# Optimization experiments

Measured on AMD Instinct MI355X. Metric: run time of the kernel, lower is better.

Reference implementation:

```python
import jax, jax.numpy as jnp
import numpy as np

B, c, H, W = 64, 3, 512, 512
R = 8  # region_num
C = B * c

def setup_inputs() -> dict:
    key = jax.random.key(0)
    k1, k2, k3 = jax.random.split(key, 3)
    return {
        "x": jax.random.normal(k1, (B, c, H, W), dtype=jnp.float32),
        "region_percentiles": jax.random.uniform(k2, (C * (R - 1),), dtype=jnp.float32),
        "proxy_percentiles": jax.random.uniform(k3, (C * R,), dtype=jnp.float32),
        "region_num": R,
    }

def reference(x, region_percentiles, proxy_percentiles, region_num):
    Bx, cx, Hx, Wx = x.shape
    Cx = Bx * cx
    xf = x.reshape(Cx, Hx * Wx)                       # (C, HW)
    min_val = xf.min(axis=1)                          # (C,)
    max_val = xf.max(axis=1)                          # (C,)
    # random percentile boundary positions per channel, sorted
    pos = (region_percentiles.reshape(Cx, region_num - 1)
           * (max_val - min_val)[:, None] + min_val[:, None])
    pos_sorted = jnp.sort(pos, axis=1)                # (C, R-1)
    # region ends: left = [min, pos...], right = [pos..., max + 1e-6]
    left = jnp.concatenate([min_val[:, None], pos_sorted], axis=1)          # (C, R)
    right = jnp.concatenate([pos_sorted, max_val[:, None] + 1e-6], axis=1)  # (C, R)
    # region id for each pixel: number of boundaries <= x (== argmax of inside-mask)
    ids = jax.vmap(lambda bnd, v: jnp.searchsorted(bnd, v, side='right'))(pos_sorted, xf)  # (C, HW) int32
    # random value inside each region, then gather per pixel
    rand_vals = left + proxy_percentiles.reshape(Cx, region_num) * (right - left)  # (C, R)
    proxy = jnp.take_along_axis(rand_vals, ids, axis=1)                            # (C, HW)
    return proxy.reshape(Bx, cx, Hx, Wx).astype(x.dtype)
```

## Files before the change

### kernel.cpp

```cpp
#include <hip/hip_runtime.h>
#include <math.h>

#pragma clang fp contract(off)

#define CCH   192
#define HW    (512*512)
#define RNUM  8
#define SPLIT 8

typedef float f32x4 __attribute__((ext_vector_type(4)));

__device__ __forceinline__ float mul_rn(float a, float b) {
    float r; asm volatile("v_mul_f32 %0, %1, %2" : "=v"(r) : "v"(a), "v"(b)); return r;
}
__device__ __forceinline__ float add_rn(float a, float b) {
    float r; asm volatile("v_add_f32 %0, %1, %2" : "=v"(r) : "v"(a), "v"(b)); return r;
}
__device__ __forceinline__ float sub_rn(float a, float b) {
    float r; asm volatile("v_sub_f32 %0, %1, %2" : "=v"(r) : "v"(a), "v"(b)); return r;
}

__global__ __launch_bounds__(256) void k_minmax(const float* __restrict__ x,
                                                float* __restrict__ ws) {
    __shared__ float smn[256], smx[256];
    const int chan = blockIdx.x / SPLIT;
    const int part = blockIdx.x % SPLIT;
    const int n4   = HW / 4 / SPLIT;

    const f32x4* px = (const f32x4*)(x + (size_t)chan * HW) + (size_t)part * n4;

    float mn = INFINITY, mx = -INFINITY;
    for (int i = threadIdx.x; i < n4; i += 256) {
        f32x4 v = px[i];
        mn = fminf(mn, fminf(fminf(v.x, v.y), fminf(v.z, v.w)));
        mx = fmaxf(mx, fmaxf(fmaxf(v.x, v.y), fmaxf(v.z, v.w)));
    }
    smn[threadIdx.x] = mn;
    smx[threadIdx.x] = mx;
    __syncthreads();
    for (int s = 128; s > 0; s >>= 1) {
        if (threadIdx.x < s) {
            smn[threadIdx.x] = fminf(smn[threadIdx.x], smn[threadIdx.x + s]);
            smx[threadIdx.x] = fmaxf(smx[threadIdx.x], smx[threadIdx.x + s]);
        }
        __syncthreads();
    }
    if (threadIdx.x == 0) {
        ws[(size_t)blockIdx.x * 2 + 0] = smn[0];
        ws[(size_t)blockIdx.x * 2 + 1] = smx[0];
    }
}

#define BLOCKS_PER_CH 16
__global__ __launch_bounds__(256) void k_apply(const float* __restrict__ x,
                                               const float* __restrict__ ws_part,
                                               const float* __restrict__ region_percentiles,
                                               const float* __restrict__ proxy_percentiles,
                                               float* __restrict__ out) {
    const int chan = blockIdx.x / BLOCKS_PER_CH;
    const int blk  = blockIdx.x % BLOCKS_PER_CH;
    const int n4   = HW / 4 / BLOCKS_PER_CH;

    __shared__ float spart[2 * SPLIT];
    __shared__ float sb[RNUM - 1];
    __shared__ float srv[RNUM];

    if (threadIdx.x < 2 * SPLIT)
        spart[threadIdx.x] = ws_part[chan * 2 * SPLIT + threadIdx.x];
    __syncthreads();

    if (threadIdx.x == 0) {
        float mn = INFINITY, mx = -INFINITY;
        #pragma unroll
        for (int p = 0; p < SPLIT; ++p) {
            mn = fminf(mn, spart[2 * p + 0]);
            mx = fmaxf(mx, spart[2 * p + 1]);
        }
        const float range = sub_rn(mx, mn);

        float pos[RNUM - 1];
        #pragma unroll
        for (int i = 0; i < RNUM - 1; ++i)
            pos[i] = add_rn(mul_rn(region_percentiles[chan * (RNUM - 1) + i], range), mn);
        for (int i = 1; i < RNUM - 1; ++i) {
            float v = pos[i];
            int j = i - 1;
            while (j >= 0 && pos[j] > v) { pos[j + 1] = pos[j]; --j; }
            pos[j + 1] = v;
        }
        #pragma unroll
        for (int i = 0; i < RNUM - 1; ++i) sb[i] = pos[i];
        #pragma unroll
        for (int i = 0; i < RNUM; ++i) {
            const float left  = (i == 0)        ? mn : pos[i - 1];
            const float right = (i == RNUM - 1) ? add_rn(mx, 1e-6f) : pos[i];
            srv[i] = add_rn(left,
                            mul_rn(proxy_percentiles[chan * RNUM + i],
                                   sub_rn(right, left)));
        }
    }
    __syncthreads();

    const float b0 = sb[0], b1 = sb[1], b2 = sb[2], b3 = sb[3];
    const float b4 = sb[4], b5 = sb[5], b6 = sb[6];

    const f32x4* px = (const f32x4*)(x   + (size_t)chan * HW) + (size_t)blk * n4;
    f32x4*       po = (f32x4*)      (out + (size_t)chan * HW) + (size_t)blk * n4;

    for (int i = threadIdx.x; i < n4; i += 256) {
        const f32x4 v = px[i];
        f32x4 o;
        {
            int id = (b0 <= v.x) + (b1 <= v.x) + (b2 <= v.x) + (b3 <= v.x)
                   + (b4 <= v.x) + (b5 <= v.x) + (b6 <= v.x);
            o.x = srv[id];
        }
        {
            int id = (b0 <= v.y) + (b1 <= v.y) + (b2 <= v.y) + (b3 <= v.y)
                   + (b4 <= v.y) + (b5 <= v.y) + (b6 <= v.y);
            o.y = srv[id];
        }
        {
            int id = (b0 <= v.z) + (b1 <= v.z) + (b2 <= v.z) + (b3 <= v.z)
                   + (b4 <= v.z) + (b5 <= v.z) + (b6 <= v.z);
            o.z = srv[id];
        }
        {
            int id = (b0 <= v.w) + (b1 <= v.w) + (b2 <= v.w) + (b3 <= v.w)
                   + (b4 <= v.w) + (b5 <= v.w) + (b6 <= v.w);
            o.w = srv[id];
        }
        __builtin_nontemporal_store(o, &po[i]);
    }
}

extern "C" void kernel_launch(void* const* d_in, const int* in_sizes, int n_in,
                              void* d_out, int out_size, void* d_ws, size_t ws_size,
                              hipStream_t stream) {
    const float* x  = (const float*)d_in[0];
    const float* rp = (const float*)d_in[1];
    const float* pp = (const float*)d_in[2];
    float* out = (float*)d_out;
    float* ws  = (float*)d_ws;

    k_minmax<<<CCH * SPLIT, 256, 0, stream>>>(x, ws);
    k_apply<<<CCH * BLOCKS_PER_CH, 256, 0, stream>>>(x, ws, rp, pp, out);
}
```

Measured before the change: 96.88 us.

## Fuse min/max and apply into one persistent kernel caching input in registers and LDS

```diff
diff --git a/kernel.cpp b/kernel.cpp
--- a/kernel.cpp
+++ b/kernel.cpp
@@ -6,7 +6,12 @@
 #define CCH   192
 #define HW    (512*512)
 #define RNUM  8
-#define SPLIT 8
+#define X4_PER_CH (HW / 4)
+#define SLAB  (X4_PER_CH / 2)
+#define PT    (SLAB / 256)
+#define NREG  80
+#define NLDS  15
+#define NUNH  (PT - NREG - NLDS)
 
 typedef float f32x4 __attribute__((ext_vector_type(4)));
 
@@ -20,68 +25,90 @@
     float r; asm volatile("v_sub_f32 %0, %1, %2" : "=v"(r) : "v"(a), "v"(b)); return r;
 }
 
-__global__ __launch_bounds__(256) void k_minmax(const float* __restrict__ x,
-                                                float* __restrict__ ws) {
+__device__ __forceinline__ float bst_sel(float v,
+    float b0, float b1, float b2, float b3, float b4, float b5, float b6,
+    float r0, float r1, float r2, float r3, float r4, float r5, float r6, float r7) {
+    return (v < b3) ? ((v < b1) ? ((v < b0) ? r0 : r1)
+                                : ((v < b2) ? r2 : r3))
+                    : ((v < b5) ? ((v < b4) ? r4 : r5)
+                                : ((v < b6) ? r6 : r7));
+}
+
+__global__ __launch_bounds__(256, 1) void k_fused(
+        const float* __restrict__ xg,
+        const float* __restrict__ region_percentiles,
+        const float* __restrict__ proxy_percentiles,
+        float* __restrict__ outg,
+        int*   __restrict__ cnt,
+        float* __restrict__ part) {
+    const int tid  = threadIdx.x;
+    const int chan = blockIdx.x >> 1;
+    const int half = blockIdx.x & 1;
+
+    const f32x4* px = (const f32x4*)xg + (size_t)chan * X4_PER_CH + (size_t)half * SLAB;
+    f32x4*       po = (f32x4*)outg     + (size_t)chan * X4_PER_CH + (size_t)half * SLAB;
+
+    __shared__ f32x4 slds[NLDS * 256];
     __shared__ float smn[256], smx[256];
-    const int chan = blockIdx.x / SPLIT;
-    const int part = blockIdx.x % SPLIT;
-    const int n4   = HW / 4 / SPLIT;
+    __shared__ float sprm[16];
 
-    const f32x4* px = (const f32x4*)(x + (size_t)chan * HW) + (size_t)part * n4;
+    f32x4 h[NREG];
+    #pragma unroll
+    for (int k = 0; k < NREG; ++k) h[k] = px[k * 256 + tid];
 
     float mn = INFINITY, mx = -INFINITY;
-    for (int i = threadIdx.x; i < n4; i += 256) {
-        f32x4 v = px[i];
-        mn = fminf(mn, fminf(fminf(v.x, v.y), fminf(v.z, v.w)));
-        mx = fmaxf(mx, fmaxf(fmaxf(v.x, v.y), fmaxf(v.z, v.w)));
+    #pragma unroll
+    for (int k = 0; k < NREG; ++k) {
+        mn = fminf(mn, fminf(fminf(h[k].x, h[k].y), fminf(h[k].z, h[k].w)));
+        mx = fmaxf(mx, fmaxf(fmaxf(h[k].x, h[k].y), fmaxf(h[k].z, h[k].w)));
     }
-    smn[threadIdx.x] = mn;
-    smx[threadIdx.x] = mx;
+    #pragma unroll
+    for (int j = 0; j < NLDS; ++j) {
+        f32x4 t = px[(NREG + j) * 256 + tid];
+        mn = fminf(mn, fminf(fminf(t.x, t.y), fminf(t.z, t.w)));
+        mx = fmaxf(mx, fmaxf(fmaxf(t.x, t.y), fmaxf(t.z, t.w)));
+        slds[j * 256 + tid] = t;
+    }
+    #pragma unroll
+    for (int j = 0; j < NUNH; ++j) {
+        f32x4 t = px[(NREG + NLDS + j) * 256 + tid];
+        mn = fminf(mn, fminf(fminf(t.x, t.y), fminf(t.z, t.w)));
+        mx = fmaxf(mx, fmaxf(fmaxf(t.x, t.y), fmaxf(t.z, t.w)));
+    }
+
+    smn[tid] = mn; smx[tid] = mx;
     __syncthreads();
     for (int s = 128; s > 0; s >>= 1) {
-        if (threadIdx.x < s) {
-            smn[threadIdx.x] = fminf(smn[threadIdx.x], smn[threadIdx.x + s]);
-            smx[threadIdx.x] = fmaxf(smx[threadIdx.x], smx[threadIdx.x + s]);
+        if (tid < s) {
+            smn[tid] = fminf(smn[tid], smn[tid + s]);
+            smx[tid] = fmaxf(smx[tid], smx[tid + s]);
         }
         __syncthreads();
     }
-    if (threadIdx.x == 0) {
-        ws[(size_t)blockIdx.x * 2 + 0] = smn[0];
-        ws[(size_t)blockIdx.x * 2 + 1] = smx[0];
-    }
-}
 
-#define BLOCKS_PER_CH 16
-__global__ __launch_bounds__(256) void k_apply(const float* __restrict__ x,
-                                               const float* __restrict__ ws_part,
-                                               const float* __restrict__ region_percentiles,
-                                               const float* __restrict__ proxy_percentiles,
-                                               float* __restrict__ out) {
-    const int chan = blockIdx.x / BLOCKS_PER_CH;
-    const int blk  = blockIdx.x % BLOCKS_PER_CH;
-    const int n4   = HW / 4 / BLOCKS_PER_CH;
+    if (tid == 0) {
+        __hip_atomic_store(&part[chan * 4 + half * 2 + 0], smn[0],
+                           __ATOMIC_RELAXED, __HIP_MEMORY_SCOPE_AGENT);
+        __hip_atomic_store(&part[chan * 4 + half * 2 + 1], smx[0],
+                           __ATOMIC_RELAXED, __HIP_MEMORY_SCOPE_AGENT);
+        __hip_atomic_fetch_add(&cnt[chan], 1,
+                               __ATOMIC_RELEASE, __HIP_MEMORY_SCOPE_AGENT);
+        while (__hip_atomic_load(&cnt[chan], __ATOMIC_ACQUIRE,
+                                 __HIP_MEMORY_SCOPE_AGENT) < 2)
+            __builtin_amdgcn_s_sleep(2);
 
-    __shared__ float spart[2 * SPLIT];
-    __shared__ float sb[RNUM - 1];
-    __shared__ float srv[RNUM];
-
-    if (threadIdx.x < 2 * SPLIT)
-        spart[threadIdx.x] = ws_part[chan * 2 * SPLIT + threadIdx.x];
-    __syncthreads();
-
-    if (threadIdx.x == 0) {
-        float mn = INFINITY, mx = -INFINITY;
-        #pragma unroll
-        for (int p = 0; p < SPLIT; ++p) {
-            mn = fminf(mn, spart[2 * p + 0]);
-            mx = fmaxf(mx, spart[2 * p + 1]);
-        }
-        const float range = sub_rn(mx, mn);
+        const float amn = __hip_atomic_load(&part[chan * 4 + 0], __ATOMIC_RELAXED, __HIP_MEMORY_SCOPE_AGENT);
+        const float amx = __hip_atomic_load(&part[chan * 4 + 1], __ATOMIC_RELAXED, __HIP_MEMORY_SCOPE_AGENT);
+        const float bmn = __hip_atomic_load(&part[chan * 4 + 2], __ATOMIC_RELAXED, __HIP_MEMORY_SCOPE_AGENT);
+        const float bmx = __hip_atomic_load(&part[chan * 4 + 3], __ATOMIC_RELAXED, __HIP_MEMORY_SCOPE_AGENT);
+        const float cmn = fminf(amn, bmn);
+        const float cmx = fmaxf(amx, bmx);
+        const float range = sub_rn(cmx, cmn);
 
         float pos[RNUM - 1];
         #pragma unroll
         for (int i = 0; i < RNUM - 1; ++i)
-            pos[i] = add_rn(mul_rn(region_percentiles[chan * (RNUM - 1) + i], range), mn);
+            pos[i] = add_rn(mul_rn(region_percentiles[chan * (RNUM - 1) + i], range), cmn);
         for (int i = 1; i < RNUM - 1; ++i) {
             float v = pos[i];
             int j = i - 1;
@@ -89,48 +116,53 @@
             pos[j + 1] = v;
         }
         #pragma unroll
-        for (int i = 0; i < RNUM - 1; ++i) sb[i] = pos[i];
+        for (int i = 0; i < RNUM - 1; ++i) sprm[i] = pos[i];
         #pragma unroll
         for (int i = 0; i < RNUM; ++i) {
-            const float left  = (i == 0)        ? mn : pos[i - 1];
-            const float right = (i == RNUM - 1) ? add_rn(mx, 1e-6f) : pos[i];
-            srv[i] = add_rn(left,
-                            mul_rn(proxy_percentiles[chan * RNUM + i],
-                                   sub_rn(right, left)));
+            const float left  = (i == 0)        ? cmn : pos[i - 1];
+            const float right = (i == RNUM - 1) ? add_rn(cmx, 1e-6f) : pos[i];
+            sprm[RNUM - 1 + i] = add_rn(left,
+                                        mul_rn(proxy_percentiles[chan * RNUM + i],
+                                               sub_rn(right, left)));
         }
     }
     __syncthreads();
 
-    const float b0 = sb[0], b1 = sb[1], b2 = sb[2], b3 = sb[3];
-    const float b4 = sb[4], b5 = sb[5], b6 = sb[6];
+    const float b0 = sprm[0], b1 = sprm[1], b2 = sprm[2], b3 = sprm[3];
+    const float b4 = sprm[4], b5 = sprm[5], b6 = sprm[6];
+    const float r0 = sprm[7],  r1 = sprm[8],  r2 = sprm[9],  r3 = sprm[10];
+    const float r4 = sprm[11], r5 = sprm[12], r6 = sprm[13], r7 = sprm[14];
 
-    const f32x4* px = (const f32x4*)(x   + (size_t)chan * HW) + (size_t)blk * n4;
-    f32x4*       po = (f32x4*)      (out + (size_t)chan * HW) + (size_t)blk * n4;
-
-    for (int i = threadIdx.x; i < n4; i += 256) {
-        const f32x4 v = px[i];
+    #pragma unroll
+    for (int j = 0; j < NUNH; ++j) {
+        const int idx = (NREG + NLDS + j) * 256 + tid;
+        const f32x4 v = px[idx];
         f32x4 o;
-        {
-            int id = (b0 <= v.x) + (b1 <= v.x) + (b2 <= v.x) + (b3 <= v.x)
-                   + (b4 <= v.x) + (b5 <= v.x) + (b6 <= v.x);
-            o.x = srv[id];
-        }
-        {
-            int id = (b0 <= v.y) + (b1 <= v.y) + (b2 <= v.y) + (b3 <= v.y)
-                   + (b4 <= v.y) + (b5 <= v.y) + (b6 <= v.y);
-            o.y = srv[id];
-        }
-        {
-            int id = (b0 <= v.z) + (b1 <= v.z) + (b2 <= v.z) + (b3 <= v.z)
-                   + (b4 <= v.z) + (b5 <= v.z) + (b6 <= v.z);
-            o.z = srv[id];
-        }
-        {
-            int id = (b0 <= v.w) + (b1 <= v.w) + (b2 <= v.w) + (b3 <= v.w)
-                   + (b4 <= v.w) + (b5 <= v.w) + (b6 <= v.w);
-            o.w = srv[id];
-        }
-        __builtin_nontemporal_store(o, &po[i]);
+        o.x = bst_sel(v.x, b0,b1,b2,b3,b4,b5,b6, r0,r1,r2,r3,r4,r5,r6,r7);
+        o.y = bst_sel(v.y, b0,b1,b2,b3,b4,b5,b6, r0,r1,r2,r3,r4,r5,r6,r7);
+        o.z = bst_sel(v.z, b0,b1,b2,b3,b4,b5,b6, r0,r1,r2,r3,r4,r5,r6,r7);
+        o.w = bst_sel(v.w, b0,b1,b2,b3,b4,b5,b6, r0,r1,r2,r3,r4,r5,r6,r7);
+        __builtin_nontemporal_store(o, &po[idx]);
+    }
+    #pragma unroll
+    for (int j = 0; j < NLDS; ++j) {
+        const f32x4 v = slds[j * 256 + tid];
+        f32x4 o;
+        o.x = bst_sel(v.x, b0,b1,b2,b3,b4,b5,b6, r0,r1,r2,r3,r4,r5,r6,r7);
+        o.y = bst_sel(v.y, b0,b1,b2,b3,b4,b5,b6, r0,r1,r2,r3,r4,r5,r6,r7);
+        o.z = bst_sel(v.z, b0,b1,b2,b3,b4,b5,b6, r0,r1,r2,r3,r4,r5,r6,r7);
+        o.w = bst_sel(v.w, b0,b1,b2,b3,b4,b5,b6, r0,r1,r2,r3,r4,r5,r6,r7);
+        __builtin_nontemporal_store(o, &po[(NREG + j) * 256 + tid]);
+    }
+    #pragma unroll
+    for (int k = 0; k < NREG; ++k) {
+        const f32x4 v = h[k];
+        f32x4 o;
+        o.x = bst_sel(v.x, b0,b1,b2,b3,b4,b5,b6, r0,r1,r2,r3,r4,r5,r6,r7);
+        o.y = bst_sel(v.y, b0,b1,b2,b3,b4,b5,b6, r0,r1,r2,r3,r4,r5,r6,r7);
+        o.z = bst_sel(v.z, b0,b1,b2,b3,b4,b5,b6, r0,r1,r2,r3,r4,r5,r6,r7);
+        o.w = bst_sel(v.w, b0,b1,b2,b3,b4,b5,b6, r0,r1,r2,r3,r4,r5,r6,r7);
+        __builtin_nontemporal_store(o, &po[k * 256 + tid]);
     }
 }
 
@@ -141,8 +173,11 @@
     const float* rp = (const float*)d_in[1];
     const float* pp = (const float*)d_in[2];
     float* out = (float*)d_out;
-    float* ws  = (float*)d_ws;
 
-    k_minmax<<<CCH * SPLIT, 256, 0, stream>>>(x, ws);
-    k_apply<<<CCH * BLOCKS_PER_CH, 256, 0, stream>>>(x, ws, rp, pp, out);
+    int*   cnt  = (int*)d_ws;
+    float* part = (float*)((char*)d_ws + 1024);
+
+    hipMemsetAsync(d_ws, 0, 1024, stream);
+
+    k_fused<<<CCH * 2, 256, 0, stream>>>(x, rp, pp, out, cnt, part);
 }
```

Measured after the change: 194.7 us. 101% more time.
